# Kernel tuning notes

Measured on AMD Instinct MI355X. Metric: run time of the kernel, lower is better.

Reference implementation:

```python
import jax, jax.numpy as jnp
import numpy as np

N_HEADS = 8
D_K = 64
SCALE = D_K ** -0.5


def setup_inputs() -> dict:
    key = jax.random.key(0)
    k1, k2, k3, k4, k5 = jax.random.split(key, 5)
    C = 512
    inner = N_HEADS * D_K  # 512
    return {
        "x": jax.random.normal(k1, (16, C, 32, 32), dtype=jnp.float32),
        "W_qkv": jax.random.normal(k2, (C, 3 * inner), dtype=jnp.float32) * (C ** -0.5),
        "b_qkv": jax.random.normal(k3, (3 * inner,), dtype=jnp.float32) * 0.02,
        "W_out": jax.random.normal(k4, (inner, C), dtype=jnp.float32) * (inner ** -0.5),
        "b_out": jax.random.normal(k5, (C,), dtype=jnp.float32) * 0.02,
    }


def reference(x, W_qkv, b_qkv, W_out, b_out):
    B, C, H, W = x.shape
    N = H * W
    xt = x.reshape(B, C, N).transpose(0, 2, 1)  # (B, N, C) tokens
    qkv = (xt @ W_qkv + b_qkv).reshape(B, N, N_HEADS, 3 * D_K)
    q, k, v = jnp.split(qkv, 3, axis=-1)  # each (B, N, H, d_k)
    # scores over key axis j; softmax along j (original dim=2 of bijh)
    attn = jnp.einsum('bihd,bjhd->bhij', q, k) * SCALE
    attn = jax.nn.softmax(attn, axis=-1)
    res = jnp.einsum('bhij,bjhd->bihd', attn, v).reshape(B, N, N_HEADS * D_K)
    res = res @ W_out + b_out + xt  # out projection + residual (note: GroupNorm unused in source forward)
    return res.transpose(0, 2, 1).reshape(B, C, H, W)
```

## Files before the change

### kernel.cpp

```cpp
#include <hip/hip_runtime.h>
#include <hip/hip_bf16.h>
#include <stdint.h>

#define N_HEADS 8
#define D_K 64
#define QSCALE (0.125f * 1.44269504088896f)

typedef __attribute__((ext_vector_type(4))) float f32x4;
typedef __attribute__((ext_vector_type(16))) float f32x16;
typedef __attribute__((ext_vector_type(8))) short bf16x8;
typedef __attribute__((ext_vector_type(4))) unsigned short u16x4;

#define AS1 __attribute__((address_space(1)))
#define AS3 __attribute__((address_space(3)))

static __device__ __forceinline__ void gload_lds16(const void* g, void* l) {
    __builtin_amdgcn_global_load_lds((const AS1 void*)g, (AS3 void*)l, 16, 0, 0);
}

static __device__ __forceinline__ __hip_bfloat16 f2bf(float f) {
    return __float2bfloat16(f);
}

static __device__ __forceinline__ unsigned short bfbits(float f) {
    return __builtin_bit_cast(unsigned short, __float2bfloat16(f));
}

static __device__ __forceinline__ uint32_t pkbf(float lo, float hi) {
    return (uint32_t)bfbits(lo) | ((uint32_t)bfbits(hi) << 16);
}

static __device__ __forceinline__ float fmax3(float a, float b, float c) {
    return fmaxf(fmaxf(a, b), c);
}

__global__ void transpose_bf16(const float* __restrict__ in,
                               __hip_bfloat16* __restrict__ out,
                               int R, int C) {
    __shared__ float tile[32][33];
    const int bz = blockIdx.z;
    const int r0 = blockIdx.y * 32, c0 = blockIdx.x * 32;
    const float* ip = in + (size_t)bz * R * C;
    __hip_bfloat16* op = out + (size_t)bz * R * C;
    const int tx = threadIdx.x, ty = threadIdx.y;
#pragma unroll
    for (int i = 0; i < 4; ++i)
        tile[ty + i * 8][tx] = ip[(size_t)(r0 + ty + i * 8) * C + c0 + tx];
    __syncthreads();
#pragma unroll
    for (int i = 0; i < 4; ++i)
        op[(size_t)(c0 + ty + i * 8) * R + r0 + tx] = f2bf(tile[tx][ty + i * 8]);
}

__device__ __forceinline__ void gemm128_tile(
    const __hip_bfloat16* __restrict__ Abase, int lda,
    const __hip_bfloat16* __restrict__ Bbase, int ldb,
    int K,
    __hip_bfloat16* Atile, __hip_bfloat16* Btile,
    f32x4 (&acc)[4][4]) {
    const int t = threadIdx.x;
    const int w = t >> 6;
    const int l = t & 63;
    const int wr = (w >> 1) * 64, wc = (w & 1) * 64;
    const int fr = l & 15, fq = l >> 4;

#pragma unroll
    for (int m = 0; m < 4; ++m)
#pragma unroll
        for (int n = 0; n < 4; ++n) acc[m][n] = (f32x4)0.f;

    for (int k0 = 0; k0 < K; k0 += 64) {
        __syncthreads();
#pragma unroll
        for (int i = 0; i < 4; ++i) {
            const int tt = t + i * 256;
            const int row = tt >> 3, c16 = tt & 7;
            const char* ga = (const char*)(Abase + (size_t)row * lda + k0) + c16 * 16;
            const char* gb = (const char*)(Bbase + (size_t)row * ldb + k0) + c16 * 16;
            char* la = (char*)Atile + w * 1024 + i * 4096;
            char* lb = (char*)Btile + w * 1024 + i * 4096;
            gload_lds16(ga, la);
            gload_lds16(gb, lb);
        }
        __syncthreads();
#pragma unroll
        for (int kb = 0; kb < 2; ++kb) {
            bf16x8 af[4], bfr[4];
#pragma unroll
            for (int m = 0; m < 4; ++m)
                af[m] = *(const bf16x8*)(Atile + (wr + m * 16 + fr) * 64 + kb * 32 + fq * 8);
#pragma unroll
            for (int n = 0; n < 4; ++n)
                bfr[n] = *(const bf16x8*)(Btile + (wc + n * 16 + fr) * 64 + kb * 32 + fq * 8);
#pragma unroll
            for (int m = 0; m < 4; ++m)
#pragma unroll
                for (int n = 0; n < 4; ++n)
                    acc[m][n] = __builtin_amdgcn_mfma_f32_16x16x32_bf16(af[m], bfr[n], acc[m][n], 0, 0, 0);
        }
    }
}

__global__ __launch_bounds__(256) void qkv_gemm(
    const __hip_bfloat16* __restrict__ xt,
    const __hip_bfloat16* __restrict__ Wqt,
    const float* __restrict__ bias,
    __hip_bfloat16* __restrict__ q_ws,
    __hip_bfloat16* __restrict__ k_ws,
    __hip_bfloat16* __restrict__ v_ws) {
    __shared__ __attribute__((aligned(16))) __hip_bfloat16 Atile[128 * 64];
    __shared__ __attribute__((aligned(16))) __hip_bfloat16 Btile[128 * 64];
    const int id0 = blockIdx.x;
    const int wg = (id0 & 7) * 192 + (id0 >> 3);
    const int tn = wg % 12;
    const int tm = (wg / 12) & 7;
    const int b  = wg / 96;
    f32x4 acc[4][4];
    gemm128_tile(xt + ((size_t)b * 1024 + tm * 128) * 512, 512,
                 Wqt + (size_t)tn * 128 * 512, 512, 512, Atile, Btile, acc);

    const int t = threadIdx.x, l = t & 63, w = t >> 6;
    const int wr = (w >> 1) * 64, wc = (w & 1) * 64, fr = l & 15, fq = l >> 4;
#pragma unroll
    for (int m = 0; m < 4; ++m) {
#pragma unroll
        for (int n = 0; n < 4; ++n) {
            const int j = tn * 128 + wc + n * 16 + fr;
            const int h = j / 192, rem = j % 192, p = rem / 64, d = rem % 64;
            const float bj = bias[j];
            const size_t bh = (size_t)b * 8 + h;
#pragma unroll
            for (int r = 0; r < 4; ++r) {
                const int nn = tm * 128 + wr + m * 16 + fq * 4 + r;
                const float v = acc[m][n][r] + bj;
                if (p == 0)      q_ws[(bh * 1024 + nn) * 64 + d] = f2bf(v * QSCALE);
                else if (p == 1) k_ws[(bh * 1024 + nn) * 64 + d] = f2bf(v);
                else             v_ws[(bh * 64 + d) * 1024 + nn] = f2bf(v);
            }
        }
    }
}

__global__ __launch_bounds__(256) void attn_kernel(
    const __hip_bfloat16* __restrict__ q_ws,
    const __hip_bfloat16* __restrict__ k_ws,
    const __hip_bfloat16* __restrict__ v_ws,
    __hip_bfloat16* __restrict__ ao) {
    __shared__ __attribute__((aligned(16))) __hip_bfloat16 KtS[3][64 * 64];
    __shared__ __attribute__((aligned(16))) __hip_bfloat16 VtS[3][64 * 64];
    __shared__ __attribute__((aligned(16))) __hip_bfloat16 Pq[4][32 * 16];

    const int id = blockIdx.x;
    const int bh = id & 127;
    const int qt = id >> 7;
    const int t = threadIdx.x, l = t & 63, w = t >> 6;
    const int lq = l & 31, hi = l >> 5;
    const int qrow = qt * 128 + w * 32 + lq;
    const int swz = (lq & 7) << 4;

    const __hip_bfloat16* qp = q_ws + ((size_t)bh * 1024 + qrow) * 64;
    bf16x8 qb[4];
#pragma unroll
    for (int s = 0; s < 4; ++s) qb[s] = *(const bf16x8*)(qp + s * 16 + hi * 8);

    f32x16 oacc[2];
    oacc[0] = (f32x16)0.f; oacc[1] = (f32x16)0.f;
    float m = -1e30f, lsum = 0.f;

    const __hip_bfloat16* kbase = k_ws + (size_t)bh * 1024 * 64;
    const __hip_bfloat16* vbase = v_ws + (size_t)bh * 64 * 1024;

    auto stage = [&](int buf, int kt2) {
#pragma unroll
        for (int i = 0; i < 2; ++i) {
            const int tt = t + i * 256;
            const int row = tt >> 3;
            const int sl = (tt & 7) ^ (row & 7);
            char* kd = (char*)&KtS[buf][0] + w * 1024 + i * 4096;
            char* vd = (char*)&VtS[buf][0] + w * 1024 + i * 4096;
            gload_lds16(kbase + (size_t)(kt2 * 64 + row) * 64 + sl * 8, kd);
            gload_lds16(vbase + (size_t)row * 1024 + kt2 * 64 + sl * 8, vd);
        }
    };

    stage(0, 0);
    stage(1, 1);
    asm volatile("s_waitcnt vmcnt(4)" ::: "memory");
    __builtin_amdgcn_s_barrier();
    __builtin_amdgcn_sched_barrier(0);

    for (int kt = 0; kt < 16; ++kt) {
        if (kt < 14) stage((kt + 2) % 3, kt + 2);

        const char* KtC = (const char*)&KtS[kt % 3][0];
        const char* VtC = (const char*)&VtS[kt % 3][0];

        f32x16 s0 = (f32x16)0.f, s1 = (f32x16)0.f;
        __builtin_amdgcn_s_setprio(1);
#pragma unroll
        for (int s = 0; s < 4; ++s) {
            const int colb = s * 32 + hi * 16;
            bf16x8 k0 = *(const bf16x8*)(KtC + ((lq * 128 + colb) ^ swz));
            bf16x8 k1 = *(const bf16x8*)(KtC + (((32 + lq) * 128 + colb) ^ swz));
            s0 = __builtin_amdgcn_mfma_f32_32x32x16_bf16(k0, qb[s], s0, 0, 0, 0);
            s1 = __builtin_amdgcn_mfma_f32_32x32x16_bf16(k1, qb[s], s1, 0, 0, 0);
        }
        __builtin_amdgcn_s_setprio(0);

        float c0 = fmax3(s0[0], s0[1], s0[2]);
        float c1 = fmax3(s0[4], s0[5], s0[6]);
        float c2 = fmax3(s0[8], s0[9], s0[10]);
        float c3 = fmax3(s0[12], s0[13], s0[14]);
        c0 = fmax3(c0, s0[3], s1[0]);
        c1 = fmax3(c1, s0[7], s1[4]);
        c2 = fmax3(c2, s0[11], s1[8]);
        c3 = fmax3(c3, s0[15], s1[12]);
        c0 = fmax3(c0, s1[1], s1[2]);
        c1 = fmax3(c1, s1[5], s1[6]);
        c2 = fmax3(c2, s1[9], s1[10]);
        c3 = fmax3(c3, s1[13], s1[14]);
        c0 = fmax3(c0, s1[3], c1);
        c2 = fmax3(c2, s1[7], s1[11]);
        float pmax = fmax3(c0, c2, fmaxf(c3, s1[15]));
        pmax = fmaxf(pmax, __shfl_xor(pmax, 32, 64));

        if (__any(pmax - m > 8.f)) {
            const float mn = fmaxf(m, pmax);
            const float corr = exp2f(m - mn);
            m = mn;
            lsum *= corr;
#pragma unroll
            for (int i = 0; i < 16; ++i) { oacc[0][i] *= corr; oacc[1][i] *= corr; }
        }

        float la0 = 0.f, la1 = 0.f, la2 = 0.f, la3 = 0.f;
#pragma unroll
        for (int i = 0; i < 16; i += 4) {
            s0[i + 0] = exp2f(s0[i + 0] - m); la0 += s0[i + 0];
            s0[i + 1] = exp2f(s0[i + 1] - m); la1 += s0[i + 1];
            s0[i + 2] = exp2f(s0[i + 2] - m); la2 += s0[i + 2];
            s0[i + 3] = exp2f(s0[i + 3] - m); la3 += s0[i + 3];
        }
#pragma unroll
        for (int i = 0; i < 16; i += 4) {
            s1[i + 0] = exp2f(s1[i + 0] - m); la0 += s1[i + 0];
            s1[i + 1] = exp2f(s1[i + 1] - m); la1 += s1[i + 1];
            s1[i + 2] = exp2f(s1[i + 2] - m); la2 += s1[i + 2];
            s1[i + 3] = exp2f(s1[i + 3] - m); la3 += s1[i + 3];
        }
        lsum += (la0 + la1) + (la2 + la3);

        char* prow = (char*)&Pq[w][0] + lq * 32;
        const int csw = ((lq >> 2) & 1) << 4;
#pragma unroll
        for (int s = 0; s < 4; ++s) {
            const int rb = (s & 1) * 8;
            uint2 W0, W1;
            if (s < 2) {
                W0.x = pkbf(s0[rb + 0], s0[rb + 1]); W0.y = pkbf(s0[rb + 2], s0[rb + 3]);
                W1.x = pkbf(s0[rb + 4], s0[rb + 5]); W1.y = pkbf(s0[rb + 6], s0[rb + 7]);
            } else {
                W0.x = pkbf(s1[rb + 0], s1[rb + 1]); W0.y = pkbf(s1[rb + 2], s1[rb + 3]);
                W1.x = pkbf(s1[rb + 4], s1[rb + 5]); W1.y = pkbf(s1[rb + 6], s1[rb + 7]);
            }
            *(uint2*)(prow + (csw ^ 0) + 8 * hi) = W0;
            *(uint2*)(prow + (csw ^ 16) + 8 * hi) = W1;
            bf16x8 pf = *(const bf16x8*)(prow + (csw ^ (hi << 4)));
            const int colb = s * 32 + hi * 16;
            bf16x8 v0 = *(const bf16x8*)(VtC + ((lq * 128 + colb) ^ swz));
            bf16x8 v1 = *(const bf16x8*)(VtC + (((32 + lq) * 128 + colb) ^ swz));
            __builtin_amdgcn_s_setprio(1);
            oacc[0] = __builtin_amdgcn_mfma_f32_32x32x16_bf16(v0, pf, oacc[0], 0, 0, 0);
            oacc[1] = __builtin_amdgcn_mfma_f32_32x32x16_bf16(v1, pf, oacc[1], 0, 0, 0);
            __builtin_amdgcn_s_setprio(0);
        }

        if (kt < 14) {
            asm volatile("s_waitcnt vmcnt(4)" ::: "memory");
            __builtin_amdgcn_s_barrier();
            __builtin_amdgcn_sched_barrier(0);
        } else if (kt == 14) {
            asm volatile("s_waitcnt vmcnt(0)" ::: "memory");
            __builtin_amdgcn_s_barrier();
            __builtin_amdgcn_sched_barrier(0);
        }
    }

    lsum += __shfl_xor(lsum, 32, 64);
    const float inv = 1.f / lsum;
    const int b = bh >> 3, h = bh & 7;
    __hip_bfloat16* aop = ao + ((size_t)b * 1024 + qrow) * 512 + h * 64;
#pragma unroll
    for (int dd = 0; dd < 2; ++dd)
#pragma unroll
        for (int rg = 0; rg < 4; ++rg) {
            u16x4 pkd;
#pragma unroll
            for (int j = 0; j < 4; ++j)
                pkd[j] = bfbits(oacc[dd][rg * 4 + j] * inv);
            const int d0 = dd * 32 + rg * 8 + hi * 4;
            *(u16x4*)(aop + d0) = pkd;
        }
}

__global__ __launch_bounds__(256) void out_gemm(
    const __hip_bfloat16* __restrict__ Wot,
    const __hip_bfloat16* __restrict__ ao,
    const float* __restrict__ bias,
    const float* __restrict__ x,
    float* __restrict__ out) {
    __shared__ __attribute__((aligned(16))) __hip_bfloat16 Atile[128 * 64];
    __shared__ __attribute__((aligned(16))) __hip_bfloat16 Btile[128 * 64];
    const int id0 = blockIdx.x;
    const int wg = (id0 & 7) * 64 + (id0 >> 3);
    const int tn = wg & 7;
    const int tc = (wg >> 3) & 3;
    const int b  = wg >> 5;
    f32x4 acc[4][4];
    gemm128_tile(Wot + (size_t)tc * 128 * 512, 512,
                 ao + ((size_t)b * 1024 + tn * 128) * 512, 512, 512, Atile, Btile, acc);

    const int t = threadIdx.x, l = t & 63, w = t >> 6;
    const int wr = (w >> 1) * 64, wc = (w & 1) * 64, fr = l & 15, fq = l >> 4;
#pragma unroll
    for (int m = 0; m < 4; ++m) {
#pragma unroll
        for (int n = 0; n < 4; ++n) {
            const int nn = tn * 128 + wc + n * 16 + fr;
#pragma unroll
            for (int r = 0; r < 4; ++r) {
                const int c = tc * 128 + wr + m * 16 + fq * 4 + r;
                const size_t idx = ((size_t)b * 512 + c) * 1024 + nn;
                out[idx] = acc[m][n][r] + bias[c] + x[idx];
            }
        }
    }
}

extern "C" void kernel_launch(void* const* d_in, const int* in_sizes, int n_in,
                              void* d_out, int out_size, void* d_ws, size_t ws_size,
                              hipStream_t stream) {
    const float* x     = (const float*)d_in[0];
    const float* W_qkv = (const float*)d_in[1];
    const float* b_qkv = (const float*)d_in[2];
    const float* W_out = (const float*)d_in[3];
    const float* b_out = (const float*)d_in[4];
    float* out = (float*)d_out;

    const int B = 16, C = 512, N = 1024, BH = B * N_HEADS;

    char* ws = (char*)d_ws;
    __hip_bfloat16* xt   = (__hip_bfloat16*)ws; ws += (size_t)B * N * C * 2;
    __hip_bfloat16* Wqt  = (__hip_bfloat16*)ws; ws += (size_t)1536 * 512 * 2;
    __hip_bfloat16* Wot  = (__hip_bfloat16*)ws; ws += (size_t)512 * 512 * 2;
    __hip_bfloat16* q_ws = (__hip_bfloat16*)ws; ws += (size_t)BH * N * 64 * 2;
    __hip_bfloat16* k_ws = (__hip_bfloat16*)ws; ws += (size_t)BH * N * 64 * 2;
    __hip_bfloat16* v_ws = (__hip_bfloat16*)ws; ws += (size_t)BH * 64 * N * 2;
    __hip_bfloat16* ao   = (__hip_bfloat16*)ws; ws += (size_t)B * N * 512 * 2;

    transpose_bf16<<<dim3(N / 32, C / 32, B), dim3(32, 8), 0, stream>>>(x, xt, C, N);
    transpose_bf16<<<dim3(1536 / 32, 512 / 32, 1), dim3(32, 8), 0, stream>>>(W_qkv, Wqt, 512, 1536);
    transpose_bf16<<<dim3(512 / 32, 512 / 32, 1), dim3(32, 8), 0, stream>>>(W_out, Wot, 512, 512);

    qkv_gemm<<<dim3(1536), 256, 0, stream>>>(xt, Wqt, b_qkv, q_ws, k_ws, v_ws);

    attn_kernel<<<dim3(1024), 256, 0, stream>>>(q_ws, k_ws, v_ws, ao);

    out_gemm<<<dim3(512), 256, 0, stream>>>(Wot, ao, b_out, x, out);
}
```

Baseline: 172.8 us.

## Double-buffer GEMM K-tiles with swizzled LDS and simplify attention to two buffers

```diff
diff --git a/kernel.cpp b/kernel.cpp
--- a/kernel.cpp
+++ b/kernel.cpp
@@ -69,35 +69,47 @@
 #pragma unroll
         for (int n = 0; n < 4; ++n) acc[m][n] = (f32x4)0.f;
 
-    for (int k0 = 0; k0 < K; k0 += 64) {
+    auto stage = [&](int buf, int k0) {
+#pragma unroll
+        for (int i = 0; i < 2; ++i) {
+            const int tt = t + i * 256;
+            const int row = tt >> 2;
+            const int sl = (tt & 3) ^ (row & 3);
+            char* la = (char*)Atile + buf * 8192 + i * 4096 + w * 1024;
+            char* lb = (char*)Btile + buf * 8192 + i * 4096 + w * 1024;
+            gload_lds16(Abase + (size_t)row * lda + k0 + sl * 8, la);
+            gload_lds16(Bbase + (size_t)row * ldb + k0 + sl * 8, lb);
+        }
+    };
+
+    const int nkt = K >> 5;
+    stage(0, 0);
+    __syncthreads();
+
+    for (int kt = 0; kt < nkt; ++kt) {
+        const int cur = kt & 1;
+        if (kt + 1 < nkt) stage(cur ^ 1, (kt + 1) * 32);
+
+        const char* Ab = (const char*)Atile + cur * 8192;
+        const char* Bb = (const char*)Btile + cur * 8192;
+        bf16x8 af[4], bfr[4];
+#pragma unroll
+        for (int m = 0; m < 4; ++m) {
+            const int row = wr + m * 16 + fr;
+            af[m] = *(const bf16x8*)(Ab + ((row * 64 + fq * 16) ^ ((row & 3) << 4)));
+        }
+#pragma unroll
+        for (int n = 0; n < 4; ++n) {
+            const int row = wc + n * 16 + fr;
+            bfr[n] = *(const bf16x8*)(Bb + ((row * 64 + fq * 16) ^ ((row & 3) << 4)));
+        }
+#pragma unroll
+        for (int m = 0; m < 4; ++m)
+#pragma unroll
+            for (int n = 0; n < 4; ++n)
+                acc[m][n] = __builtin_amdgcn_mfma_f32_16x16x32_bf16(af[m], bfr[n], acc[m][n], 0, 0, 0);
+
         __syncthreads();
-#pragma unroll
-        for (int i = 0; i < 4; ++i) {
-            const int tt = t + i * 256;
-            const int row = tt >> 3, c16 = tt & 7;
-            const char* ga = (const char*)(Abase + (size_t)row * lda + k0) + c16 * 16;
-            const char* gb = (const char*)(Bbase + (size_t)row * ldb + k0) + c16 * 16;
-            char* la = (char*)Atile + w * 1024 + i * 4096;
-            char* lb = (char*)Btile + w * 1024 + i * 4096;
-            gload_lds16(ga, la);
-            gload_lds16(gb, lb);
-        }
-        __syncthreads();
-#pragma unroll
-        for (int kb = 0; kb < 2; ++kb) {
-            bf16x8 af[4], bfr[4];
-#pragma unroll
-            for (int m = 0; m < 4; ++m)
-                af[m] = *(const bf16x8*)(Atile + (wr + m * 16 + fr) * 64 + kb * 32 + fq * 8);
-#pragma unroll
-            for (int n = 0; n < 4; ++n)
-                bfr[n] = *(const bf16x8*)(Btile + (wc + n * 16 + fr) * 64 + kb * 32 + fq * 8);
-#pragma unroll
-            for (int m = 0; m < 4; ++m)
-#pragma unroll
-                for (int n = 0; n < 4; ++n)
-                    acc[m][n] = __builtin_amdgcn_mfma_f32_16x16x32_bf16(af[m], bfr[n], acc[m][n], 0, 0, 0);
-        }
     }
 }
 
@@ -108,8 +120,8 @@
     __hip_bfloat16* __restrict__ q_ws,
     __hip_bfloat16* __restrict__ k_ws,
     __hip_bfloat16* __restrict__ v_ws) {
-    __shared__ __attribute__((aligned(16))) __hip_bfloat16 Atile[128 * 64];
-    __shared__ __attribute__((aligned(16))) __hip_bfloat16 Btile[128 * 64];
+    __shared__ __attribute__((aligned(16))) __hip_bfloat16 Atile[2][128 * 32];
+    __shared__ __attribute__((aligned(16))) __hip_bfloat16 Btile[2][128 * 32];
     const int id0 = blockIdx.x;
     const int wg = (id0 & 7) * 192 + (id0 >> 3);
     const int tn = wg % 12;
@@ -117,7 +129,8 @@
     const int b  = wg / 96;
     f32x4 acc[4][4];
     gemm128_tile(xt + ((size_t)b * 1024 + tm * 128) * 512, 512,
-                 Wqt + (size_t)tn * 128 * 512, 512, 512, Atile, Btile, acc);
+                 Wqt + (size_t)tn * 128 * 512, 512, 512,
+                 &Atile[0][0], &Btile[0][0], acc);
 
     const int t = threadIdx.x, l = t & 63, w = t >> 6;
     const int wr = (w >> 1) * 64, wc = (w & 1) * 64, fr = l & 15, fq = l >> 4;
@@ -146,8 +159,8 @@
     const __hip_bfloat16* __restrict__ k_ws,
     const __hip_bfloat16* __restrict__ v_ws,
     __hip_bfloat16* __restrict__ ao) {
-    __shared__ __attribute__((aligned(16))) __hip_bfloat16 KtS[3][64 * 64];
-    __shared__ __attribute__((aligned(16))) __hip_bfloat16 VtS[3][64 * 64];
+    __shared__ __attribute__((aligned(16))) __hip_bfloat16 KtS[2][64 * 64];
+    __shared__ __attribute__((aligned(16))) __hip_bfloat16 VtS[2][64 * 64];
     __shared__ __attribute__((aligned(16))) __hip_bfloat16 Pq[4][32 * 16];
 
     const int id = blockIdx.x;
@@ -184,16 +197,14 @@
     };
 
     stage(0, 0);
-    stage(1, 1);
-    asm volatile("s_waitcnt vmcnt(4)" ::: "memory");
-    __builtin_amdgcn_s_barrier();
-    __builtin_amdgcn_sched_barrier(0);
+    __syncthreads();
 
     for (int kt = 0; kt < 16; ++kt) {
-        if (kt < 14) stage((kt + 2) % 3, kt + 2);
-
-        const char* KtC = (const char*)&KtS[kt % 3][0];
-        const char* VtC = (const char*)&VtS[kt % 3][0];
+        const int cur = kt & 1;
+        if (kt < 15) stage(cur ^ 1, kt + 1);
+
+        const char* KtC = (const char*)&KtS[cur][0];
+        const char* VtC = (const char*)&VtS[cur][0];
 
         f32x16 s0 = (f32x16)0.f, s1 = (f32x16)0.f;
         __builtin_amdgcn_s_setprio(1);
@@ -275,15 +286,7 @@
             __builtin_amdgcn_s_setprio(0);
         }
 
-        if (kt < 14) {
-            asm volatile("s_waitcnt vmcnt(4)" ::: "memory");
-            __builtin_amdgcn_s_barrier();
-            __builtin_amdgcn_sched_barrier(0);
-        } else if (kt == 14) {
-            asm volatile("s_waitcnt vmcnt(0)" ::: "memory");
-            __builtin_amdgcn_s_barrier();
-            __builtin_amdgcn_sched_barrier(0);
-        }
+        __syncthreads();
     }
 
     lsum += __shfl_xor(lsum, 32, 64);
@@ -309,8 +312,8 @@
     const float* __restrict__ bias,
     const float* __restrict__ x,
     float* __restrict__ out) {
-    __shared__ __attribute__((aligned(16))) __hip_bfloat16 Atile[128 * 64];
-    __shared__ __attribute__((aligned(16))) __hip_bfloat16 Btile[128 * 64];
+    __shared__ __attribute__((aligned(16))) __hip_bfloat16 Atile[2][128 * 32];
+    __shared__ __attribute__((aligned(16))) __hip_bfloat16 Btile[2][128 * 32];
     const int id0 = blockIdx.x;
     const int wg = (id0 & 7) * 64 + (id0 >> 3);
     const int tn = wg & 7;
@@ -318,7 +321,8 @@
     const int b  = wg >> 5;
     f32x4 acc[4][4];
     gemm128_tile(Wot + (size_t)tc * 128 * 512, 512,
-                 ao + ((size_t)b * 1024 + tn * 128) * 512, 512, 512, Atile, Btile, acc);
+                 ao + ((size_t)b * 1024 + tn * 128) * 512, 512, 512,
+                 &Atile[0][0], &Btile[0][0], acc);
 
     const int t = threadIdx.x, l = t & 63, w = t >> 6;
     const int wr = (w >> 1) * 64, wc = (w & 1) * 64, fr = l & 15, fq = l >> 4;
```

Result: faster. 168.3 us (-2.6%).
